# Performance work log

Measured on AMD Instinct MI355X. Metric: run time of the kernel, lower is better.

## Reference

```python
import jax, jax.numpy as jnp
import numpy as np

B, T, D, U, S = 128, 256, 256, 256, 3
GRID_SIZE, SPLINE_ORDER = 5, 3
COEFFS = GRID_SIZE + SPLINE_ORDER  # 8


def _grid():
    h = 2.0 / GRID_SIZE  # grid_range = (-1, 1)
    return -1.0 + h * jnp.arange(-SPLINE_ORDER, GRID_SIZE + SPLINE_ORDER + 1, dtype=jnp.float32)


def _b_splines(x, grid):
    # Cox-de Boor recursion. x: (B, D) -> (B, D, COEFFS)
    x = x[..., None]
    b = ((x >= grid[:-1]) & (x < grid[1:])).astype(x.dtype)
    for k in range(1, SPLINE_ORDER + 1):
        b = (x - grid[:-(k + 1)]) / (grid[k:-1] - grid[:-(k + 1)]) * b[..., :-1] \
          + (grid[k + 1:] - x) / (grid[k + 1:] - grid[1:-k]) * b[..., 1:]
    return b


def setup_inputs() -> dict:
    key = jax.random.key(0)
    ks = jax.random.split(key, 8)
    x = jax.random.normal(ks[0], (B, T, D), jnp.float32)
    kernel = jax.random.normal(ks[1], (D, 3 * U), jnp.float32) / np.float32(np.sqrt(D))
    recurrent_kernel = jax.random.normal(ks[2], (U, 3 * U), jnp.float32) / np.float32(np.sqrt(U))
    # unit_forget_bias: gate order (i, f, c)
    bias = jnp.zeros((3 * U,), jnp.float32).at[U:2 * U].set(1.0)
    sub_tkan_kernel = jax.random.normal(ks[3], (S, 2), jnp.float32)
    sub_tkan_recurrent_kernel = jax.random.normal(ks[4], (S, 2 * D), jnp.float32) / np.float32(np.sqrt(D))
    aggregated_weight = jax.random.normal(ks[5], (S, U), jnp.float32)
    aggregated_bias = jnp.zeros((U,), jnp.float32)
    kan_base_weight = jax.random.normal(ks[6], (S, D, 1), jnp.float32) / np.float32(np.sqrt(D))
    kan_spline_weight = jax.random.normal(ks[7], (S, D, COEFFS, 1), jnp.float32) * 0.1
    return dict(x=x, kernel=kernel, recurrent_kernel=recurrent_kernel, bias=bias,
                sub_tkan_kernel=sub_tkan_kernel,
                sub_tkan_recurrent_kernel=sub_tkan_recurrent_kernel,
                aggregated_weight=aggregated_weight, aggregated_bias=aggregated_bias,
                kan_base_weight=kan_base_weight, kan_spline_weight=kan_spline_weight)


def reference(x, kernel, recurrent_kernel, bias, sub_tkan_kernel,
              sub_tkan_recurrent_kernel, aggregated_weight, aggregated_bias,
              kan_base_weight, kan_spline_weight):
    grid = _grid()
    b, t, d = x.shape
    u = kernel.shape[1] // 3
    s = sub_tkan_kernel.shape[0]
    skx = sub_tkan_recurrent_kernel[:, :d]    # (S, D) input scale
    skh = sub_tkan_recurrent_kernel[:, d:]    # (S, D) sub-state scale
    srk_h = sub_tkan_kernel[:, 0][:, None, None]  # (S,1,1)
    srk_x = sub_tkan_kernel[:, 1][:, None, None]  # (S,1,1)

    def kan(xin, bw, sw):
        # xin (B, D), bw (D, 1), sw (D, COEFFS, 1) -> (B, 1)
        base = jax.nn.silu(xin) @ bw
        spline = jnp.einsum('bdc,dco->bo', _b_splines(xin, grid), sw)
        return base + spline

    kan_v = jax.vmap(kan)  # over the S sub-layers

    def step(carry, x_t):
        h, c, sub = carry  # (B,U), (B,U), (S,B,1)
        z = x_t @ kernel + h @ recurrent_kernel + bias  # (B, 3U)
        zi, zf, zc = jnp.split(z, 3, axis=1)
        i = jax.nn.sigmoid(zi)
        f = jax.nn.sigmoid(zf)
        c_new = f * c + i * jnp.tanh(zc)
        # KAN sub-layers: mix input with scalar sub-state, evaluate spline net
        agg_in = x_t[None] * skx[:, None, :] + sub * skh[:, None, :]  # (S,B,D)
        sub_out = kan_v(agg_in, kan_base_weight, kan_spline_weight)   # (S,B,1)
        sub_new = srk_h * sub_out + srk_x * sub                       # (S,B,1)
        # output gate from aggregated sub-layer outputs
        o = jax.nn.sigmoid(sub_out[..., 0].T @ aggregated_weight + aggregated_bias)  # (B,U)
        h_new = o * jnp.tanh(c_new)
        return (h_new, c_new, sub_new), h_new

    init = (jnp.zeros((b, u), x.dtype), jnp.zeros((b, u), x.dtype),
            jnp.zeros((s, b, 1), x.dtype))
    _, ys = jax.lax.scan(step, init, jnp.swapaxes(x, 0, 1))
    return jnp.swapaxes(ys, 0, 1)  # (B, T, U) full sequence of hidden states
```

## Files before the change

### kernel.cpp

```cpp
#include <hip/hip_runtime.h>

#define B_  128
#define T_  256
#define D_  256
#define U_  256
#define TU  768
#define TC  64
#define NC  (T_/TC)

__device__ __forceinline__ float sigm(float x) { return 1.f / (1.f + __expf(-x)); }

__device__ __forceinline__ float tanh_fast(float x) {
    float e = __expf(2.f * x);
    return 1.f - 2.f / (e + 1.f);
}

__device__ __forceinline__ float spline_eval(float x, const float* __restrict__ ksw_lds, int u) {
    float xc = (x + 2.2f) * 2.5f;
    float fj = floorf(xc);
    int   j  = (int)fj;
    float tl = xc - fj;
    float t2 = tl * tl, t3 = t2 * tl;
    float om = 1.f - tl;
    const float S = 1.f / 6.f;
    float w0 = om * om * om * S;
    float w1 = (3.f * t3 - 6.f * t2 + 4.f) * S;
    float w2 = (-3.f * t3 + 3.f * t2 + 3.f * tl + 1.f) * S;
    float w3 = t3 * S;
    bool  v  = (j >= 0) && (j <= 10);
    float r  = 0.f;
#pragma unroll
    for (int k = 0; k < 4; ++k) {
        int   m  = j - 3 + k;
        bool  ok = v && (m >= 0) && (m <= 7);
        int   mc = min(max(m, 0), 7);
        float wk = (k == 0) ? w0 : (k == 1) ? w1 : (k == 2) ? w2 : w3;
        float cf = ksw_lds[u * 9 + mc];
        r += ok ? wk * cf : 0.f;
    }
    return r;
}

__global__ void k0_init(float* __restrict__ wh, float* __restrict__ wc,
                        float* __restrict__ wsub, float* __restrict__ xh) {
    int i = blockIdx.x * 256 + threadIdx.x;
    wh[i] = 0.f;
    wc[i] = 0.f;
    ((int*)xh)[i]         = 1;
    ((int*)xh)[i + 32768] = 1;
    if (i < 3 * B_) wsub[i] = 0.f;
}

__global__ __launch_bounds__(256) void k1_gemm(const float* __restrict__ X,
                                               const float* __restrict__ Km,
                                               const float* __restrict__ bias,
                                               float* __restrict__ A, int t0) {
    __shared__ float Xs[16][68];
    __shared__ float Ks[16][68];
    const int bm  = blockIdx.x * 64;
    const int bn  = blockIdx.y * 64;
    const int tid = threadIdx.x;
    const int ty = tid >> 4, tx = tid & 15;

    const int lr  = tid >> 2;
    const int lk4 = (tid & 3) * 4;
    const int rr  = bm + lr;
    const int b   = rr >> 6;
    const int tl  = rr & 63;
    const float* xrow = X + (size_t)(b * T_ + t0 + tl) * D_;

    const int kr  = tid >> 4;
    const int kn4 = (tid & 15) * 4;

    float acc[4][4] = {};
    for (int kb = 0; kb < 256; kb += 16) {
        float4 xv = *(const float4*)(xrow + kb + lk4);
        Xs[lk4 + 0][lr] = xv.x;
        Xs[lk4 + 1][lr] = xv.y;
        Xs[lk4 + 2][lr] = xv.z;
        Xs[lk4 + 3][lr] = xv.w;
        *(float4*)&Ks[kr][kn4] = *(const float4*)(Km + (size_t)(kb + kr) * TU + bn + kn4);
        __syncthreads();
#pragma unroll
        for (int k = 0; k < 16; ++k) {
            float4 av = *(float4*)&Xs[k][ty * 4];
            float4 bv = *(float4*)&Ks[k][tx * 4];
            acc[0][0] += av.x * bv.x; acc[0][1] += av.x * bv.y; acc[0][2] += av.x * bv.z; acc[0][3] += av.x * bv.w;
            acc[1][0] += av.y * bv.x; acc[1][1] += av.y * bv.y; acc[1][2] += av.y * bv.z; acc[1][3] += av.y * bv.w;
            acc[2][0] += av.z * bv.x; acc[2][1] += av.z * bv.y; acc[2][2] += av.z * bv.z; acc[2][3] += av.z * bv.w;
            acc[3][0] += av.w * bv.x; acc[3][1] += av.w * bv.y; acc[3][2] += av.w * bv.z; acc[3][3] += av.w * bv.w;
        }
        __syncthreads();
    }
    float4 bv = *(const float4*)(bias + bn + tx * 4);
#pragma unroll
    for (int i = 0; i < 4; ++i) {
        float4 o;
        o.x = acc[i][0] + bv.x; o.y = acc[i][1] + bv.y;
        o.z = acc[i][2] + bv.z; o.w = acc[i][3] + bv.w;
        *(float4*)(A + (size_t)(bm + ty * 4 + i) * TU + bn + tx * 4) = o;
    }
}

__global__ __launch_bounds__(512, 2)
void k2_rec(const float* __restrict__ A,
            const float* __restrict__ X,
            const float* __restrict__ R,
            const float* __restrict__ stk,
            const float* __restrict__ strk,
            const float* __restrict__ aggw,
            const float* __restrict__ aggb,
            const float* __restrict__ kbw,
            const float* __restrict__ ksw,
            float* __restrict__ out,
            float* __restrict__ ws_h,
            float* __restrict__ ws_c,
            float* __restrict__ ws_sub,
            float* __restrict__ xh,
            int t0) {
    __shared__ float hs[256];
    __shared__ float xs[256];
    __shared__ float zred[8][64][3];
    __shared__ float kred[768];
    __shared__ float so_l[3];
    __shared__ float subs[3];
    __shared__ float st2[6];
    __shared__ float hhist[TC][128];
    __shared__ float ksw_lds[768 * 9];

    const int tid  = threadIdx.x;
    const int lane = tid & 63;
    const int w    = tid >> 6;
    const int p    = w & 3;
    const int c    = ((w >> 2) << 6) | lane;
    const int b    = blockIdx.x & 127;
    const int r    = blockIdx.x >> 7;
    const int ui   = r * 128 + c;
    const bool pstate = (p == 0);

    float Rf[3][64];
#pragma unroll
    for (int g = 0; g < 3; ++g)
#pragma unroll
        for (int uu = 0; uu < 64; ++uu)
            Rf[g][uu] = R[(size_t)(p * 64 + uu) * TU + g * 256 + ui];

    const int s0 = tid >> 8, d0 = tid & 255;
    const float skx0 = strk[s0 * 512 + d0];
    const float skh0 = strk[s0 * 512 + 256 + d0];
    const float bw0  = kbw[tid];
    int u1i = -1;
    if (tid >= 64 && tid < 256)       u1i = tid - 64;
    else if (tid >= 320 && tid < 384) u1i = tid - 128;
    float skx1 = 0.f, skh1 = 0.f, bw1 = 0.f;
    if (u1i >= 0) {
        skx1 = strk[2 * 512 + u1i];
        skh1 = strk[2 * 512 + 256 + u1i];
        bw1  = kbw[512 + u1i];
    }

    const float aw0 = aggw[ui], aw1 = aggw[256 + ui], aw2 = aggw[512 + ui], ab = aggb[ui];
    float c_reg = ws_c[b * 256 + ui];

    for (int i = tid; i < 768 * 8; i += 512) ksw_lds[(i >> 3) * 9 + (i & 7)] = ksw[i];
    if (tid < 256) hs[tid] = ws_h[b * 256 + tid];
    if (tid < 256) xs[tid] = X[((size_t)b * T_ + t0) * D_ + tid];
    if (tid < 3)   subs[tid] = ws_sub[b * 3 + tid];
    if (tid < 6)   st2[tid] = stk[tid];

    float az0 = 0.f, az1 = 0.f, az2 = 0.f;
    float xv = 0.f;
    __syncthreads();

    for (int tl = 0; tl < TC; ++tl) {
        const int t = t0 + tl;

        if (pstate) {
            if (tl > 0) {
                float z0 = az0, z1 = az1, z2 = az2;
#pragma unroll
                for (int q = 0; q < 4; ++q) {
                    z0 += zred[w + q][lane][0];
                    z1 += zred[w + q][lane][1];
                    z2 += zred[w + q][lane][2];
                }
                float ig = sigm(z0);
                float fg = sigm(z1);
                c_reg = fg * c_reg + ig * tanh_fast(z2);
                float og = sigm(so_l[0] * aw0 + so_l[1] * aw1 + so_l[2] * aw2 + ab);
                float hn = og * tanh_fast(c_reg);
                hs[ui] = hn;
                hhist[tl - 1][c] = hn;
                unsigned hb = (__float_as_uint(hn) & ~1u) | (unsigned)(((t - 1) >> 1) & 1);
                __hip_atomic_store((unsigned*)&xh[((size_t)b * 2 + ((t - 1) & 1)) * 256 + ui],
                                   hb, __ATOMIC_RELAXED, __HIP_MEMORY_SCOPE_SYSTEM);
            }
            const float* Ap = A + ((size_t)b * TC + tl) * TU + ui;
            az0 = Ap[0]; az1 = Ap[256]; az2 = Ap[512];
        }
        if (u1i >= 0) {
            int tn = (t + 1 < T_) ? t + 1 : t;
            xv = X[((size_t)b * T_ + tn) * D_ + u1i];
        }
        {
            float a0 = xs[d0] * skx0 + subs[s0] * skh0;
            kred[tid] = a0 * sigm(a0) * bw0 + spline_eval(a0, ksw_lds, tid);
        }
        if (u1i >= 0) {
            float a1 = xs[u1i] * skx1 + subs[2] * skh1;
            kred[512 + u1i] = a1 * sigm(a1) * bw1 + spline_eval(a1, ksw_lds, 512 + u1i);
        }
        if (tl > 0 && tid >= 384) {
            const int uidx = (1 - r) * 128 + (tid - 384);
            const unsigned expect = (unsigned)(((t - 1) >> 1) & 1);
            const unsigned* src = (const unsigned*)&xh[((size_t)b * 2 + ((t - 1) & 1)) * 256 + uidx];
            unsigned v;
            do {
                v = __hip_atomic_load(src, __ATOMIC_RELAXED, __HIP_MEMORY_SCOPE_SYSTEM);
            } while ((v & 1u) != expect);
            hs[uidx] = __uint_as_float(v);
        }
        __syncthreads();

        {
            const float* hp = &hs[p * 64];
            float a0 = 0.f, a1 = 0.f, a2 = 0.f;
#pragma unroll
            for (int j = 0; j < 16; ++j) {
                float4 h4 = *(const float4*)(hp + j * 4);
                a0 = fmaf(h4.x, Rf[0][j * 4 + 0], a0);
                a1 = fmaf(h4.x, Rf[1][j * 4 + 0], a1);
                a2 = fmaf(h4.x, Rf[2][j * 4 + 0], a2);
                a0 = fmaf(h4.y, Rf[0][j * 4 + 1], a0);
                a1 = fmaf(h4.y, Rf[1][j * 4 + 1], a1);
                a2 = fmaf(h4.y, Rf[2][j * 4 + 1], a2);
                a0 = fmaf(h4.z, Rf[0][j * 4 + 2], a0);
                a1 = fmaf(h4.z, Rf[1][j * 4 + 2], a1);
                a2 = fmaf(h4.z, Rf[2][j * 4 + 2], a2);
                a0 = fmaf(h4.w, Rf[0][j * 4 + 3], a0);
                a1 = fmaf(h4.w, Rf[1][j * 4 + 3], a1);
                a2 = fmaf(h4.w, Rf[2][j * 4 + 3], a2);
            }
            zred[w][lane][0] = a0;
            zred[w][lane][1] = a1;
            zred[w][lane][2] = a2;
        }
        if (w < 3) {
            float v = kred[w * 256 + lane] + kred[w * 256 + 64 + lane]
                    + kred[w * 256 + 128 + lane] + kred[w * 256 + 192 + lane];
#pragma unroll
            for (int m = 32; m > 0; m >>= 1) v += __shfl_xor(v, m, 64);
            if (lane == 0) {
                so_l[w] = v;
                subs[w] = st2[w * 2] * v + st2[w * 2 + 1] * subs[w];
            }
        }
        if (u1i >= 0) xs[u1i] = xv;
        __syncthreads();
    }

    if (pstate) {
        float z0 = az0, z1 = az1, z2 = az2;
#pragma unroll
        for (int q = 0; q < 4; ++q) {
            z0 += zred[w + q][lane][0];
            z1 += zred[w + q][lane][1];
            z2 += zred[w + q][lane][2];
        }
        float ig = sigm(z0);
        float fg = sigm(z1);
        c_reg = fg * c_reg + ig * tanh_fast(z2);
        float og = sigm(so_l[0] * aw0 + so_l[1] * aw1 + so_l[2] * aw2 + ab);
        float hn = og * tanh_fast(c_reg);
        hhist[TC - 1][c] = hn;
        ws_h[b * 256 + ui] = hn;
        ws_c[b * 256 + ui] = c_reg;
        {
            const int s = t0 + TC - 1;
            unsigned hb = (__float_as_uint(hn) & ~1u) | (unsigned)(((s) >> 1) & 1);
            __hip_atomic_store((unsigned*)&xh[((size_t)b * 2 + (s & 1)) * 256 + ui],
                               hb, __ATOMIC_RELAXED, __HIP_MEMORY_SCOPE_SYSTEM);
        }
    }
    __syncthreads();
    for (int i = tid; i < TC * 128; i += 512) {
        int tl = i >> 7, cc = i & 127;
        out[((size_t)b * T_ + t0 + tl) * U_ + r * 128 + cc] = hhist[tl][cc];
    }
    if (tid < 3) ws_sub[b * 3 + tid] = subs[tid];
}

extern "C" void kernel_launch(void* const* d_in, const int* in_sizes, int n_in,
                              void* d_out, int out_size, void* d_ws, size_t ws_size,
                              hipStream_t stream) {
    const float* x    = (const float*)d_in[0];
    const float* Kmat = (const float*)d_in[1];
    const float* R    = (const float*)d_in[2];
    const float* bias = (const float*)d_in[3];
    const float* stk  = (const float*)d_in[4];
    const float* strk = (const float*)d_in[5];
    const float* aggw = (const float*)d_in[6];
    const float* aggb = (const float*)d_in[7];
    const float* kbw  = (const float*)d_in[8];
    const float* ksw  = (const float*)d_in[9];
    float* out = (float*)d_out;

    float* ws   = (float*)d_ws;
    float* A    = ws;
    float* wh   = A + (size_t)B_ * TC * TU;
    float* wc   = wh + B_ * U_;
    float* wsub = wc + B_ * U_;
    float* xh   = wsub + 512;

    k0_init<<<dim3(B_), dim3(256), 0, stream>>>(wh, wc, wsub, xh);
    for (int ci = 0; ci < NC; ++ci) {
        k1_gemm<<<dim3((B_ * TC) / 64, TU / 64), dim3(256), 0, stream>>>(x, Kmat, bias, A, ci * TC);
        k2_rec<<<dim3(2 * B_), dim3(512), 0, stream>>>(A, x, R, stk, strk, aggw, aggb, kbw, ksw,
                                                       out, wh, wc, wsub, xh, ci * TC);
    }
}
```

Baseline: 802.1 us.

## Widen GEMM tiles, reorder recurrent spin-wait, split FMA chains

The input-projection GEMM now uses 64x128 tiles with a 4x8 register tile per thread, so each staged X value is reused across more outputs and half as many blocks are launched. In the recurrent kernel, the spin-wait on the partner block's hidden state moves to the top of each step. The h publish is issued before the local LDS writes so the other block sees it sooner. The recurrent dot product is split into two accumulator chains to shorten the FMA dependency latency. Extra accumulator registers may lower occupancy, and the earlier spin can delay the KAN work of the polling waves.

After: 950.6 us. 18.5% more time.

```diff
diff --git a/kernel.cpp b/kernel.cpp
--- a/kernel.cpp
+++ b/kernel.cpp
@@ -56,49 +56,56 @@
                                                const float* __restrict__ bias,
                                                float* __restrict__ A, int t0) {
     __shared__ float Xs[16][68];
-    __shared__ float Ks[16][68];
+    __shared__ float Ks[16][132];
+    const int tid = threadIdx.x;
     const int bm  = blockIdx.x * 64;
-    const int bn  = blockIdx.y * 64;
-    const int tid = threadIdx.x;
+    const int bn  = blockIdx.y * 128;
+
     const int ty = tid >> 4, tx = tid & 15;
-
-    const int lr  = tid >> 2;
-    const int lk4 = (tid & 3) * 4;
-    const int rr  = bm + lr;
-    const int b   = rr >> 6;
-    const int tl  = rr & 63;
-    const float* xrow = X + (size_t)(b * T_ + t0 + tl) * D_;
-
-    const int kr  = tid >> 4;
-    const int kn4 = (tid & 15) * 4;
-
-    float acc[4][4] = {};
+    const int m0 = ty * 4,  n0 = tx * 4;
+
+    const int xr = tid & 63, kq = (tid >> 6) * 4;
+    const int rr = bm + xr;
+    const float* xrow = X + (size_t)((rr >> 6) * T_ + t0 + (rr & 63)) * D_;
+
+    const int kr = tid >> 4, nq = (tid & 15) * 8;
+
+    float acc[4][8] = {};
     for (int kb = 0; kb < 256; kb += 16) {
-        float4 xv = *(const float4*)(xrow + kb + lk4);
-        Xs[lk4 + 0][lr] = xv.x;
-        Xs[lk4 + 1][lr] = xv.y;
-        Xs[lk4 + 2][lr] = xv.z;
-        Xs[lk4 + 3][lr] = xv.w;
-        *(float4*)&Ks[kr][kn4] = *(const float4*)(Km + (size_t)(kb + kr) * TU + bn + kn4);
+        float4 xv = *(const float4*)(xrow + kb + kq);
+        Xs[kq + 0][xr] = xv.x;
+        Xs[kq + 1][xr] = xv.y;
+        Xs[kq + 2][xr] = xv.z;
+        Xs[kq + 3][xr] = xv.w;
+        *(float4*)&Ks[kr][nq]     = *(const float4*)(Km + (size_t)(kb + kr) * TU + bn + nq);
+        *(float4*)&Ks[kr][nq + 4] = *(const float4*)(Km + (size_t)(kb + kr) * TU + bn + nq + 4);
         __syncthreads();
 #pragma unroll
         for (int k = 0; k < 16; ++k) {
-            float4 av = *(float4*)&Xs[k][ty * 4];
-            float4 bv = *(float4*)&Ks[k][tx * 4];
-            acc[0][0] += av.x * bv.x; acc[0][1] += av.x * bv.y; acc[0][2] += av.x * bv.z; acc[0][3] += av.x * bv.w;
-            acc[1][0] += av.y * bv.x; acc[1][1] += av.y * bv.y; acc[1][2] += av.y * bv.z; acc[1][3] += av.y * bv.w;
-            acc[2][0] += av.z * bv.x; acc[2][1] += av.z * bv.y; acc[2][2] += av.z * bv.z; acc[2][3] += av.z * bv.w;
-            acc[3][0] += av.w * bv.x; acc[3][1] += av.w * bv.y; acc[3][2] += av.w * bv.z; acc[3][3] += av.w * bv.w;
+            float4 av = *(float4*)&Xs[k][m0];
+            float4 b0 = *(float4*)&Ks[k][n0];
+            float4 b1 = *(float4*)&Ks[k][64 + n0];
+            float a[4] = {av.x, av.y, av.z, av.w};
+            float bb[8] = {b0.x, b0.y, b0.z, b0.w, b1.x, b1.y, b1.z, b1.w};
+#pragma unroll
+            for (int i = 0; i < 4; ++i)
+#pragma unroll
+                for (int j = 0; j < 8; ++j)
+                    acc[i][j] = fmaf(a[i], bb[j], acc[i][j]);
         }
         __syncthreads();
     }
-    float4 bv = *(const float4*)(bias + bn + tx * 4);
+    float4 bv0 = *(const float4*)(bias + bn + n0);
+    float4 bv1 = *(const float4*)(bias + bn + 64 + n0);
 #pragma unroll
     for (int i = 0; i < 4; ++i) {
-        float4 o;
-        o.x = acc[i][0] + bv.x; o.y = acc[i][1] + bv.y;
-        o.z = acc[i][2] + bv.z; o.w = acc[i][3] + bv.w;
-        *(float4*)(A + (size_t)(bm + ty * 4 + i) * TU + bn + tx * 4) = o;
+        float4 o0, o1;
+        o0.x = acc[i][0] + bv0.x; o0.y = acc[i][1] + bv0.y;
+        o0.z = acc[i][2] + bv0.z; o0.w = acc[i][3] + bv0.w;
+        o1.x = acc[i][4] + bv1.x; o1.y = acc[i][5] + bv1.y;
+        o1.z = acc[i][6] + bv1.z; o1.w = acc[i][7] + bv1.w;
+        *(float4*)(A + (size_t)(bm + m0 + i) * TU + bn + n0)      = o0;
+        *(float4*)(A + (size_t)(bm + m0 + i) * TU + bn + 64 + n0) = o1;
     }
 }
 
@@ -175,6 +182,16 @@
     for (int tl = 0; tl < TC; ++tl) {
         const int t = t0 + tl;
 
+        if (tl > 0 && tid >= 384) {
+            const int uidx = (1 - r) * 128 + (tid - 384);
+            const unsigned expect = (unsigned)(((t - 1) >> 1) & 1);
+            const unsigned* src = (const unsigned*)&xh[((size_t)b * 2 + ((t - 1) & 1)) * 256 + uidx];
+            unsigned v;
+            do {
+                v = __hip_atomic_load(src, __ATOMIC_RELAXED, __HIP_MEMORY_SCOPE_SYSTEM);
+            } while ((v & 1u) != expect);
+            hs[uidx] = __uint_as_float(v);
+        }
         if (pstate) {
             if (tl > 0) {
                 float z0 = az0, z1 = az1, z2 = az2;
@@ -189,11 +206,11 @@
                 c_reg = fg * c_reg + ig * tanh_fast(z2);
                 float og = sigm(so_l[0] * aw0 + so_l[1] * aw1 + so_l[2] * aw2 + ab);
                 float hn = og * tanh_fast(c_reg);
-                hs[ui] = hn;
-                hhist[tl - 1][c] = hn;
                 unsigned hb = (__float_as_uint(hn) & ~1u) | (unsigned)(((t - 1) >> 1) & 1);
                 __hip_atomic_store((unsigned*)&xh[((size_t)b * 2 + ((t - 1) & 1)) * 256 + ui],
                                    hb, __ATOMIC_RELAXED, __HIP_MEMORY_SCOPE_SYSTEM);
+                hs[ui] = hn;
+                hhist[tl - 1][c] = hn;
             }
             const float* Ap = A + ((size_t)b * TC + tl) * TU + ui;
             az0 = Ap[0]; az1 = Ap[256]; az2 = Ap[512];
@@ -210,40 +227,44 @@
             float a1 = xs[u1i] * skx1 + subs[2] * skh1;
             kred[512 + u1i] = a1 * sigm(a1) * bw1 + spline_eval(a1, ksw_lds, 512 + u1i);
         }
-        if (tl > 0 && tid >= 384) {
-            const int uidx = (1 - r) * 128 + (tid - 384);
-            const unsigned expect = (unsigned)(((t - 1) >> 1) & 1);
-            const unsigned* src = (const unsigned*)&xh[((size_t)b * 2 + ((t - 1) & 1)) * 256 + uidx];
-            unsigned v;
-            do {
-                v = __hip_atomic_load(src, __ATOMIC_RELAXED, __HIP_MEMORY_SCOPE_SYSTEM);
-            } while ((v & 1u) != expect);
-            hs[uidx] = __uint_as_float(v);
-        }
         __syncthreads();
 
         {
             const float* hp = &hs[p * 64];
             float a0 = 0.f, a1 = 0.f, a2 = 0.f;
-#pragma unroll
-            for (int j = 0; j < 16; ++j) {
-                float4 h4 = *(const float4*)(hp + j * 4);
-                a0 = fmaf(h4.x, Rf[0][j * 4 + 0], a0);
-                a1 = fmaf(h4.x, Rf[1][j * 4 + 0], a1);
-                a2 = fmaf(h4.x, Rf[2][j * 4 + 0], a2);
-                a0 = fmaf(h4.y, Rf[0][j * 4 + 1], a0);
-                a1 = fmaf(h4.y, Rf[1][j * 4 + 1], a1);
-                a2 = fmaf(h4.y, Rf[2][j * 4 + 1], a2);
-                a0 = fmaf(h4.z, Rf[0][j * 4 + 2], a0);
-                a1 = fmaf(h4.z, Rf[1][j * 4 + 2], a1);
-                a2 = fmaf(h4.z, Rf[2][j * 4 + 2], a2);
-                a0 = fmaf(h4.w, Rf[0][j * 4 + 3], a0);
-                a1 = fmaf(h4.w, Rf[1][j * 4 + 3], a1);
-                a2 = fmaf(h4.w, Rf[2][j * 4 + 3], a2);
+            float b0 = 0.f, b1 = 0.f, b2 = 0.f;
+#pragma unroll
+            for (int j = 0; j < 8; ++j) {
+                float4 h4 = *(const float4*)(hp + j * 8);
+                float4 h5 = *(const float4*)(hp + j * 8 + 4);
+                a0 = fmaf(h4.x, Rf[0][j * 8 + 0], a0);
+                a1 = fmaf(h4.x, Rf[1][j * 8 + 0], a1);
+                a2 = fmaf(h4.x, Rf[2][j * 8 + 0], a2);
+                b0 = fmaf(h4.y, Rf[0][j * 8 + 1], b0);
+                b1 = fmaf(h4.y, Rf[1][j * 8 + 1], b1);
+                b2 = fmaf(h4.y, Rf[2][j * 8 + 1], b2);
+                a0 = fmaf(h4.z, Rf[0][j * 8 + 2], a0);
+                a1 = fmaf(h4.z, Rf[1][j * 8 + 2], a1);
+                a2 = fmaf(h4.z, Rf[2][j * 8 + 2], a2);
+                b0 = fmaf(h4.w, Rf[0][j * 8 + 3], b0);
+                b1 = fmaf(h4.w, Rf[1][j * 8 + 3], b1);
+                b2 = fmaf(h4.w, Rf[2][j * 8 + 3], b2);
+                a0 = fmaf(h5.x, Rf[0][j * 8 + 4], a0);
+                a1 = fmaf(h5.x, Rf[1][j * 8 + 4], a1);
+                a2 = fmaf(h5.x, Rf[2][j * 8 + 4], a2);
+                b0 = fmaf(h5.y, Rf[0][j * 8 + 5], b0);
+                b1 = fmaf(h5.y, Rf[1][j * 8 + 5], b1);
+                b2 = fmaf(h5.y, Rf[2][j * 8 + 5], b2);
+                a0 = fmaf(h5.z, Rf[0][j * 8 + 6], a0);
+                a1 = fmaf(h5.z, Rf[1][j * 8 + 6], a1);
+                a2 = fmaf(h5.z, Rf[2][j * 8 + 6], a2);
+                b0 = fmaf(h5.w, Rf[0][j * 8 + 7], b0);
+                b1 = fmaf(h5.w, Rf[1][j * 8 + 7], b1);
+                b2 = fmaf(h5.w, Rf[2][j * 8 + 7], b2);
             }
-            zred[w][lane][0] = a0;
-            zred[w][lane][1] = a1;
-            zred[w][lane][2] = a2;
+            zred[w][lane][0] = a0 + b0;
+            zred[w][lane][1] = a1 + b1;
+            zred[w][lane][2] = a2 + b2;
         }
         if (w < 3) {
             float v = kred[w * 256 + lane] + kred[w * 256 + 64 + lane]
@@ -314,7 +335,7 @@
 
     k0_init<<<dim3(B_), dim3(256), 0, stream>>>(wh, wc, wsub, xh);
     for (int ci = 0; ci < NC; ++ci) {
-        k1_gemm<<<dim3((B_ * TC) / 64, TU / 64), dim3(256), 0, stream>>>(x, Kmat, bias, A, ci * TC);
+        k1_gemm<<<dim3((B_ * TC) / 64, TU / 128), dim3(256), 0, stream>>>(x, Kmat, bias, A, ci * TC);
         k2_rec<<<dim3(2 * B_), dim3(512), 0, stream>>>(A, x, R, stk, strk, aggw, aggb, kbw, ksw,
                                                        out, wh, wc, wsub, xh, ci * TC);
     }
```
